# Kernel tuning notes

Measured on AMD Instinct MI355X. Metric: run time of the kernel, lower is better.

## Reference

```python
import jax, jax.numpy as jnp
import numpy as np
from jax import lax

FEAT_STRIDE = 16
RATIOS = np.array([0.5, 1.0, 2.0], np.float32)
SCALES = np.array([8.0, 16.0, 32.0], np.float32)
PRE_NMS, POST_NMS = 6000, 300
NMS_THRESH, MIN_SIZE, SCALE = 0.7, 16.0, 1.0


def anchor_base():
    py = px = FEAT_STRIDE / 2.0
    base = np.zeros((9, 4), np.float32)
    for i, r in enumerate(RATIOS):
        for j, s in enumerate(SCALES):
            h = FEAT_STRIDE * s * np.sqrt(r)
            w = FEAT_STRIDE * s * np.sqrt(1.0 / r)
            base[i * 3 + j] = [px - w / 2.0, py - h / 2.0, px + w / 2.0, py + h / 2.0]
    return jnp.asarray(base)


def all_anchors(h, w):
    base = anchor_base()  # (9,4)
    sy = jnp.arange(h, dtype=jnp.float32) * FEAT_STRIDE
    sx = jnp.arange(w, dtype=jnp.float32) * FEAT_STRIDE
    yy, xx = jnp.meshgrid(sy, sx, indexing='ij')
    shift = jnp.stack([xx.ravel(), yy.ravel(), xx.ravel(), yy.ravel()], axis=1)  # (hw,4)
    return (shift[:, None, :] + base[None, :, :]).reshape(-1, 4)  # (hw*9,4)


def conv2d(x, w, b):
    y = lax.conv_general_dilated(x, w, (1, 1), 'SAME',
                                 dimension_numbers=('NCHW', 'OIHW', 'NCHW'))
    return y + b[None, :, None, None]


def loc2bbox(anchor, loc):
    aw = anchor[:, 2] - anchor[:, 0]
    ah = anchor[:, 3] - anchor[:, 1]
    ax = anchor[:, 0] + 0.5 * aw
    ay = anchor[:, 1] + 0.5 * ah
    cx = loc[:, 0] * aw + ax
    cy = loc[:, 1] * ah + ay
    w = jnp.exp(loc[:, 2]) * aw
    h = jnp.exp(loc[:, 3]) * ah
    return jnp.stack([cx - 0.5 * w, cy - 0.5 * h, cx + 0.5 * w, cy + 0.5 * h], axis=1)


def nms_fixed(boxes, scores):
    # top pre_nms by score, then greedy sequential NMS with fixed shapes
    s, order = lax.top_k(scores, PRE_NMS)
    b = boxes[order]
    areas = (b[:, 2] - b[:, 0]) * (b[:, 3] - b[:, 1])
    idx = jnp.arange(PRE_NMS)

    def body(i, keep):
        xx1 = jnp.maximum(b[i, 0], b[:, 0])
        yy1 = jnp.maximum(b[i, 1], b[:, 1])
        xx2 = jnp.minimum(b[i, 2], b[:, 2])
        yy2 = jnp.minimum(b[i, 3], b[:, 3])
        inter = jnp.clip(xx2 - xx1, 0.0) * jnp.clip(yy2 - yy1, 0.0)
        iou = inter / (areas[i] + areas - inter + 1e-9)
        suppress = (iou > NMS_THRESH) & (idx > i) & keep[i]
        return keep & ~suppress

    keep = lax.fori_loop(0, PRE_NMS, body, jnp.isfinite(s))
    vals, sel = lax.top_k(jnp.where(keep, s, -jnp.inf), POST_NMS)
    roi = b[sel]
    return jnp.where(jnp.isfinite(vals)[:, None], roi, 0.0)  # (POST_NMS,4)


def proposal(loc, fg, anchor, img_h, img_w):
    roi = loc2bbox(anchor, loc)
    roi = jnp.stack([jnp.clip(roi[:, 0], 0.0, img_w), jnp.clip(roi[:, 1], 0.0, img_h),
                     jnp.clip(roi[:, 2], 0.0, img_w), jnp.clip(roi[:, 3], 0.0, img_h)], axis=1)
    ms = MIN_SIZE * SCALE
    valid = ((roi[:, 2] - roi[:, 0]) >= ms) & ((roi[:, 3] - roi[:, 1]) >= ms)
    return nms_fixed(roi, jnp.where(valid, fg, -jnp.inf))


def setup_inputs() -> dict:
    key = jax.random.key(0)
    ks = jax.random.split(key, 4)
    return {
        'x': jax.random.normal(ks[0], (8, 512, 50, 76), jnp.float32),
        'conv1_w': jax.random.normal(ks[1], (512, 512, 3, 3), jnp.float32) * 0.01,
        'conv1_b': jnp.zeros((512,), jnp.float32),
        'score_w': jax.random.normal(ks[2], (18, 512, 1, 1), jnp.float32) * 0.01,
        'score_b': jnp.zeros((18,), jnp.float32),
        'loc_w': jax.random.normal(ks[3], (36, 512, 1, 1), jnp.float32) * 0.01,
        'loc_b': jnp.zeros((36,), jnp.float32),
        'img_h': 800,
        'img_w': 1216,
    }


def reference(x, conv1_w, conv1_b, score_w, score_b, loc_w, loc_b, img_h, img_w):
    b, c, h, w = x.shape
    anchor = all_anchors(h, w)  # (h*w*9,4)
    feat = jax.nn.relu(conv2d(x, conv1_w, conv1_b))
    rpn_locs = conv2d(feat, loc_w, loc_b).transpose(0, 2, 3, 1).reshape(b, -1, 4)
    rpn_scores = conv2d(feat, score_w, score_b).transpose(0, 2, 3, 1)
    sm = jax.nn.softmax(rpn_scores.reshape(b, h, w, 9, 2), axis=4)
    fg = sm[..., 1].reshape(b, -1)
    rpn_scores = rpn_scores.reshape(b, -1, 2)
    rois = jax.vmap(lambda l, f: proposal(l, f, anchor, float(img_h), float(img_w)))(rpn_locs, fg)
    rois = rois.reshape(-1, 4)  # (b*POST_NMS,4)
    return rpn_locs, rpn_scores, rois, anchor
```

## Files before the change

kernel.cpp:

```cpp
#include <hip/hip_runtime.h>
#include <stdint.h>
#include <math.h>

typedef unsigned long long u64;
typedef unsigned int u32;
typedef _Float16 half8 __attribute__((ext_vector_type(8)));
typedef float f32x4 __attribute__((ext_vector_type(4)));

#define CC   512
#define HH   50
#define WW2  76
#define PP   3800
#define NB   8
#define NA   34200
#define PRE  6000
#define POST 300
#define MWORDS 96
#define NPAD 8192
#define SHALF 4096
#define SCHUNK 1069


__device__ __forceinline__ u32 skey(float f) {
    u32 u = __float_as_uint(f);
    return (u & 0x80000000u) ? ~u : (u | 0x80000000u);
}

__device__ __forceinline__ float4 anchor_at(int p, int a) {
    const float rv[3] = {0.5f, 1.0f, 2.0f};
    const float sv[3] = {8.0f, 16.0f, 32.0f};
    int ri = a / 3, si = a % 3;
    float s16 = 16.0f * sv[si];
    float hh = s16 * sqrtf(rv[ri]);
    float ww = s16 * sqrtf(1.0f / rv[ri]);
    float bx1 = 8.0f - 0.5f * ww, by1 = 8.0f - 0.5f * hh;
    float bx2 = 8.0f + 0.5f * ww, by2 = 8.0f + 0.5f * hh;
    float sx = (float)((p % WW2) * 16);
    float sy = (float)((p / WW2) * 16);
    return make_float4(sx + bx1, sy + by1, sx + bx2, sy + by2);
}

__device__ __forceinline__ int lds_slot(int m, int j) {
    return (((m >> 4) * 64) + ((m & 15) ^ ((4 * (j & 1)) | (8 * (j >> 1)))) + (j << 4)) << 3;
}

__global__ void k_split_x(const float* __restrict__ x, _Float16* __restrict__ xh,
                          _Float16* __restrict__ xl) {
    __shared__ float S[32][33];
    int zim = blockIdx.z;
    int p0 = blockIdx.x * 32, c0 = blockIdx.y * 32;
    int tx = threadIdx.x, ty0 = threadIdx.y;
    const float* xi = x + (size_t)zim * CC * PP;
#pragma unroll
    for (int yy = 0; yy < 32; yy += 8) {
        int cty = c0 + ty0 + yy, ptx = p0 + tx;
        S[ty0 + yy][tx] = (ptx < PP) ? xi[(size_t)cty * PP + ptx] : 0.f;
    }
    __syncthreads();
#pragma unroll
    for (int yy = 0; yy < 32; yy += 8) {
        int p = p0 + ty0 + yy;
        if (p < PP) {
            float v = S[tx][ty0 + yy];
            _Float16 h = (_Float16)v;
            float r = v - (float)h;
            size_t o = (size_t)(zim * PP + p) * 512 + c0 + tx;
            xh[o] = h;
            xl[o] = (_Float16)(r * 2048.0f);
        }
    }
}

__global__ void k_split_w(const float* __restrict__ w, _Float16* __restrict__ wh,
                          _Float16* __restrict__ wl) {
    __shared__ float S[4608];
    int co = blockIdx.x;
    for (int t = threadIdx.x; t < 4608; t += 256) S[t] = w[(size_t)co * 4608 + t];
    __syncthreads();
    int g = co >> 4, nlo = co & 15;
    for (int e = threadIdx.x; e < 4608; e += 256) {
        int cc = e / 9, idx = e - cc * 9;
        float v = S[cc * 9 + idx];
        _Float16 h = (_Float16)v;
        float r = v - (float)h;
        int kk = (cc >> 5) * 9 + idx;
        int lane = ((cc >> 3) & 3) * 16 + nlo;
        int j = cc & 7;
        size_t d = (((size_t)g * 144 + kk) * 64 + lane) * 8 + j;
        wh[d] = h;
        wl[d] = (_Float16)(r * 2048.0f);
    }
}

__global__ void k_split_w2(const float* __restrict__ lw, const float* __restrict__ sw,
                           _Float16* __restrict__ wh2, _Float16* __restrict__ wl2) {
    int row = blockIdx.x, k = threadIdx.x;
    float v = (row < 36) ? lw[row * 512 + k] : (row < 54 ? sw[(row - 36) * 512 + k] : 0.f);
    _Float16 h = (_Float16)v;
    float r = v - (float)h;
    wh2[row * 512 + k] = h;
    wl2[row * 512 + k] = (_Float16)(r * 2048.0f);
}

__global__ __launch_bounds__(256, 2) void k_conv(
    const _Float16* __restrict__ xh, const _Float16* __restrict__ xl,
    const _Float16* __restrict__ whF, const _Float16* __restrict__ wlF,
    const float* __restrict__ bias, _Float16* __restrict__ fh,
    _Float16* __restrict__ fl, int imgbase)
{
    __shared__ _Float16 lds[2 * 8192];
    const int tid = threadIdx.x;
    const int L = blockIdx.x;
    const int X = L & 7, q = L >> 3;
    const int nt = X & 3;
    const int zim = (X >> 2) * 2 + (q >= 30 ? 1 : 0);
    const int mt = q - (q >= 30 ? 30 : 0);
    const int m0 = mt * 128, n0 = nt * 128;
    const _Float16* xhi = xh + (size_t)zim * CC * PP;
    const _Float16* xlo = xl + (size_t)zim * CC * PP;

    const int mA0 = tid >> 2, jA0 = tid & 3;
    const int mA1 = 64 + (tid >> 2);

    f32x4 acc[4][4], acc2[4][4];
#pragma unroll
    for (int i = 0; i < 4; ++i)
#pragma unroll
        for (int j = 0; j < 4; ++j) {
            acc[i][j] = f32x4{0.f, 0.f, 0.f, 0.f};
            acc2[i][j] = f32x4{0.f, 0.f, 0.f, 0.f};
        }

    uint4 pa0h, pa0l, pa1h, pa1l;

    auto ld_a = [&](int m, int idx, int c0, uint4& vh, uint4& vl) {
        int dy = idx / 3 - 1, dx = idx % 3 - 1;
        int p = m0 + m;
        int px = p % 76, py = p / 76;
        bool av = (p < PP) && ((unsigned)(py + dy) < 50u) && ((unsigned)(px + dx) < 76u);
        if (av) {
            size_t off = (size_t)(p + dy * 76 + dx) * 512 + c0 + jA0 * 8;
            vh = *(const uint4*)(xhi + off);
            vl = *(const uint4*)(xlo + off);
        } else {
            vh = make_uint4(0, 0, 0, 0);
            vl = make_uint4(0, 0, 0, 0);
        }
    };
    auto stage_load = [&](int kk) {
        int c9 = kk / 9;
        int idx = kk - c9 * 9;
        int c0 = c9 << 5;
        ld_a(mA0, idx, c0, pa0h, pa0l);
        ld_a(mA1, idx, c0, pa1h, pa1l);
    };
    const int sl0 = lds_slot(mA0, jA0);
    const int sl1 = lds_slot(mA1, jA0);
    auto stage_write = [&](int buf) {
        _Float16* Lp = lds + buf * 8192;
        *(uint4*)(Lp + sl0)        = pa0h;
        *(uint4*)(Lp + 4096 + sl0) = pa0l;
        *(uint4*)(Lp + sl1)        = pa1h;
        *(uint4*)(Lp + 4096 + sl1) = pa1l;
    };

    const int lane = tid & 63, wave = tid >> 6;
    const int wm = wave & 1, wn = wave >> 1;
    const int jr = lane >> 4;
    const int rd_off = (((lane & 15) ^ ((4 * (jr & 1)) | (8 * (jr >> 1)))) + (jr << 4)) << 3;
    const int g0 = nt * 8 + wn * 4;
    const size_t lane8 = (size_t)lane * 8;

    half8 b0h[4], b0l[4], b1h[4], b1l[4];
    auto load_b = [&](int kk, half8* bh_, half8* bl_) {
#pragma unroll
        for (int ni = 0; ni < 4; ++ni) {
            size_t off = (((size_t)(g0 + ni) * 144 + kk) * 64) * 8 + lane8;
            bh_[ni] = *(const half8*)(whF + off);
            bl_[ni] = *(const half8*)(wlF + off);
        }
    };

    auto compute = [&](int buf, const half8* bh, const half8* bl) {
        const _Float16* Lp = lds + buf * 8192;
        half8 ah[4], al[4];
#pragma unroll
        for (int mi = 0; mi < 4; ++mi) {
            int slot = (((wm * 4 + mi) * 64) << 3) + rd_off;
            ah[mi] = *(const half8*)(Lp + slot);
            al[mi] = *(const half8*)(Lp + 4096 + slot);
        }
#pragma unroll
        for (int ni = 0; ni < 4; ++ni) {
#pragma unroll
            for (int mi = 0; mi < 4; ++mi) {
                acc[mi][ni]  = __builtin_amdgcn_mfma_f32_16x16x32_f16(ah[mi], bh[ni], acc[mi][ni], 0, 0, 0);
                acc2[mi][ni] = __builtin_amdgcn_mfma_f32_16x16x32_f16(ah[mi], bl[ni], acc2[mi][ni], 0, 0, 0);
                acc2[mi][ni] = __builtin_amdgcn_mfma_f32_16x16x32_f16(al[mi], bh[ni], acc2[mi][ni], 0, 0, 0);
            }
        }
    };

    stage_load(0);
    stage_write(0);
    load_b(0, b0h, b0l);
    __syncthreads();
    for (int kk = 0; kk < 144; kk += 2) {
        stage_load(kk + 1);
        load_b(kk + 1, b1h, b1l);
        compute(0, b0h, b0l);
        stage_write(1);
        __syncthreads();
        if (kk + 2 < 144) {
            stage_load(kk + 2);
            load_b(kk + 2, b0h, b0l);
        }
        compute(1, b1h, b1l);
        if (kk + 2 < 144) stage_write(0);
        __syncthreads();
    }

    const int qq = lane >> 4, cl = lane & 15;
    const size_t rowbase = (size_t)(imgbase + zim) * PP;
#pragma unroll
    for (int ni = 0; ni < 4; ++ni) {
        int n = n0 + (wn * 4 + ni) * 16 + cl;
        float bs = bias[n];
#pragma unroll
        for (int mi = 0; mi < 4; ++mi) {
            int mb = m0 + (wm * 4 + mi) * 16 + qq * 4;
            if (mb < PP) {
#pragma unroll
                for (int r = 0; r < 4; ++r) {
                    float v = fmaxf(acc[mi][ni][r] + acc2[mi][ni][r] * (1.f / 2048.f) + bs, 0.f);
                    _Float16 h = (_Float16)v;
                    float rr = v - (float)h;
                    size_t o = (rowbase + mb + r) * 512 + n;
                    fh[o] = h;
                    fl[o] = (_Float16)(rr * 2048.0f);
                }
            }
        }
    }
}

__global__ __launch_bounds__(256) void k_hgemm_post(
    const _Float16* __restrict__ fh, const _Float16* __restrict__ fl,
    const _Float16* __restrict__ wh2, const _Float16* __restrict__ wl2,
    const float* __restrict__ lb, const float* __restrict__ sbias,
    const int* __restrict__ imh_p, const int* __restrict__ imw_p,
    float* __restrict__ out0, float* __restrict__ out1,
    float* __restrict__ boxes, float* __restrict__ scores,
    float* __restrict__ out3)
{
    const int img = blockIdx.y;
    const int p0 = blockIdx.x * 64;
    const int wave = threadIdx.x >> 6, lane = threadIdx.x & 63;
    const int q8 = (lane >> 4) * 8;
    int arow = img * PP + p0 + wave * 16 + (lane & 15);
    if (arow >= NB * PP) arow = NB * PP - 1;
    const _Float16* fhp = fh + (size_t)arow * 512 + q8;
    const _Float16* flp = fl + (size_t)arow * 512 + q8;
    const _Float16* bhp = wh2 + (size_t)(lane & 15) * 512 + q8;
    const _Float16* blp = wl2 + (size_t)(lane & 15) * 512 + q8;

    f32x4 acc[4], acc2[4];
#pragma unroll
    for (int j = 0; j < 4; ++j) {
        acc[j] = f32x4{0.f, 0.f, 0.f, 0.f};
        acc2[j] = f32x4{0.f, 0.f, 0.f, 0.f};
    }

#pragma unroll 4
    for (int k0 = 0; k0 < 512; k0 += 32) {
        half8 ah = *(const half8*)(fhp + k0);
        half8 al = *(const half8*)(flp + k0);
#pragma unroll
        for (int nf = 0; nf < 4; ++nf) {
            half8 bh = *(const half8*)(bhp + (size_t)nf * 16 * 512 + k0);
            half8 bl = *(const half8*)(blp + (size_t)nf * 16 * 512 + k0);
            acc[nf]  = __builtin_amdgcn_mfma_f32_16x16x32_f16(ah, bh, acc[nf], 0, 0, 0);
            acc2[nf] = __builtin_amdgcn_mfma_f32_16x16x32_f16(ah, bl, acc2[nf], 0, 0, 0);
            acc2[nf] = __builtin_amdgcn_mfma_f32_16x16x32_f16(al, bh, acc2[nf], 0, 0, 0);
        }
    }

    __shared__ float Ls[64][68];
    const int q = lane >> 4, cl = lane & 15;
#pragma unroll
    for (int nf = 0; nf < 4; ++nf) {
        int n = nf * 16 + cl;
        float bs = (n < 36) ? lb[n] : (n < 54 ? sbias[n - 36] : 0.f);
#pragma unroll
        for (int r = 0; r < 4; ++r) {
            int ml = wave * 16 + q * 4 + r;
            Ls[ml][n] = acc[nf][r] + acc2[nf][r] * (1.f / 2048.f) + bs;
        }
    }
    __syncthreads();

    const float fimh = (float)(*imh_p), fimw = (float)(*imw_p);
    for (int task = threadIdx.x; task < 576; task += 256) {
        int pl = task / 9, a = task - pl * 9;
        int p = p0 + pl;
        if (p >= PP) continue;
        float4 loc = *(const float4*)&Ls[pl][a * 4];
        float2 sc = make_float2(Ls[pl][36 + a * 2], Ls[pl][36 + a * 2 + 1]);
        size_t ai = (size_t)img * NA + (size_t)p * 9 + a;
        *(float4*)&out0[ai * 4] = loc;
        *(float2*)&out1[ai * 2] = sc;
        float mx = fmaxf(sc.x, sc.y);
        float e0 = expf(sc.x - mx), e1 = expf(sc.y - mx);
        float fg = e1 / (e0 + e1);
        float4 an = anchor_at(p, a);
        if (img == 0) ((float4*)out3)[p * 9 + a] = an;
        float aw = an.z - an.x, ah = an.w - an.y;
        float ax = an.x + 0.5f * aw, ay = an.y + 0.5f * ah;
        float cx = loc.x * aw + ax;
        float cy = loc.y * ah + ay;
        float wb = expf(loc.z) * aw, hb = expf(loc.w) * ah;
        float x1 = cx - 0.5f * wb, y1 = cy - 0.5f * hb;
        float x2 = cx + 0.5f * wb, y2 = cy + 0.5f * hb;
        x1 = fminf(fmaxf(x1, 0.f), fimw);
        x2 = fminf(fmaxf(x2, 0.f), fimw);
        y1 = fminf(fmaxf(y1, 0.f), fimh);
        y2 = fminf(fmaxf(y2, 0.f), fimh);
        bool valid = ((x2 - x1) >= 16.0f) && ((y2 - y1) >= 16.0f);
        ((float4*)boxes)[ai] = make_float4(x1, y1, x2, y2);
        scores[ai] = valid ? fg : -INFINITY;
    }
}


__global__ __launch_bounds__(256) void k_sel_hist(
    const float* __restrict__ scores, u32* __restrict__ ghist,
    const u32* __restrict__ gpref, int sh, int pass)
{
    __shared__ u32 wh[4][256];
    const int img = blockIdx.y, blk = blockIdx.x;
    const int tid = threadIdx.x, wv = tid >> 6;
#pragma unroll
    for (int w = 0; w < 4; ++w) wh[w][tid] = 0;
    __syncthreads();
    const u32 pmask = (pass == 0) ? 0u : (0xFFFFFFFFu << (sh + 8));
    const u32 pref = (pass == 0) ? 0u : gpref[img];
    const float4* sc4 = (const float4*)(scores + (size_t)img * NA);
    const int e40 = blk * SCHUNK;
    const int e41 = min(e40 + SCHUNK, NA / 4);
    for (int e4 = e40 + tid; e4 < e41; e4 += 256) {
        float4 s4 = sc4[e4];
        u32 kv[4] = {skey(s4.x), skey(s4.y), skey(s4.z), skey(s4.w)};
#pragma unroll
        for (int v = 0; v < 4; ++v)
            if ((kv[v] & pmask) == pref) atomicAdd(&wh[wv][(kv[v] >> sh) & 255u], 1u);
    }
    __syncthreads();
    u32 s = wh[0][tid] + wh[1][tid] + wh[2][tid] + wh[3][tid];
    if (s) atomicAdd(&ghist[img * 256 + tid], s);
}

__global__ __launch_bounds__(256) void k_sel_scan(
    u32* __restrict__ ghist, u32* __restrict__ gpref, u32* __restrict__ grem,
    int sh, int pass)
{
    __shared__ u32 A[256];
    __shared__ int s_d;
    const int img = blockIdx.x, t = threadIdx.x;
    u32 h = ghist[img * 256 + t];
    A[t] = h;
    if (t == 0) s_d = 0;
    __syncthreads();
    for (int off = 1; off < 256; off <<= 1) {
        u32 v = A[t] + ((t + off < 256) ? A[t + off] : 0u);
        __syncthreads();
        A[t] = v;
        __syncthreads();
    }
    const u32 rem = (pass == 0) ? (u32)PRE : grem[img];
    if (A[t] >= rem) atomicMax(&s_d, t);
    __syncthreads();
    if (t == 0) {
        int d = s_d;
        u32 snext = (d < 255) ? A[d + 1] : 0u;
        u32 pv = (pass == 0) ? 0u : gpref[img];
        gpref[img] = pv | ((u32)d << sh);
        grem[img] = rem - snext;
    }
    ghist[img * 256 + t] = 0;
}

__global__ __launch_bounds__(256) void k_sel_collect(
    const float* __restrict__ scores, const u32* __restrict__ gpref,
    u32* __restrict__ gccnt, u64* __restrict__ arr)
{
    __shared__ u64 lst[4288];
    __shared__ u32 s_c, s_base;
    const int img = blockIdx.y, blk = blockIdx.x;
    const int tid = threadIdx.x, lane = tid & 63;
    if (tid == 0) s_c = 0;
    __syncthreads();
    const u32 T = gpref[img];
    const float4* sc4 = (const float4*)(scores + (size_t)img * NA);
    const int e40 = blk * SCHUNK;
    const int e41 = min(e40 + SCHUNK, NA / 4);
    for (int e4 = e40 + tid; e4 < e41; e4 += 256) {
        float4 s4 = sc4[e4];
        u32 ks[4] = {skey(s4.x), skey(s4.y), skey(s4.z), skey(s4.w)};
#pragma unroll
        for (int v = 0; v < 4; ++v) {
            bool take = ks[v] >= T;
            u64 bal = __ballot(take);
            if (bal) {
                int leader = __builtin_ctzll(bal);
                u32 base = 0;
                if (lane == leader) base = atomicAdd(&s_c, (u32)__popcll(bal));
                base = (u32)__shfl((int)base, leader);
                if (take)
                    lst[base + (u32)__popcll(bal & ((1ull << lane) - 1ull))] =
                        ((u64)ks[v] << 32) | (u64)(~(u32)(e4 * 4 + v));
            }
        }
    }
    __syncthreads();
    if (tid == 0) s_base = atomicAdd(&gccnt[img], s_c);
    __syncthreads();
    const u32 base = s_base, c = s_c;
    u64* ar = arr + (size_t)img * NPAD;
    for (u32 t = tid; t < c; t += 256) {
        u32 pos = base + t;
        if (pos < NPAD) ar[pos] = lst[t];
    }
}

__global__ __launch_bounds__(1024) void k_sel_sort2(
    u64* __restrict__ arr, const u32* __restrict__ gccnt)
{
    __shared__ u64 a[SHALF];
    const int img = blockIdx.y, half = blockIdx.x;
    const int tid = threadIdx.x;
    u32 n = gccnt[img]; if (n > NPAD) n = NPAD;
    u64* ar = arr + (size_t)img * NPAD + (size_t)half * SHALF;
    const int base = half * SHALF;
    for (int t = tid; t < SHALF; t += 1024)
        a[t] = ((u32)(base + t) < n) ? ar[t] : 0ull;
    for (u32 size = 2; size <= SHALF; size <<= 1) {
        for (u32 stride = size >> 1; stride > 0; stride >>= 1) {
            __syncthreads();
            for (u32 t2 = tid; t2 < SHALF / 2; t2 += 1024) {
                u32 i = 2 * t2 - (t2 & (stride - 1));
                u32 j = i + stride;
                u64 x = a[i], y = a[j];
                bool desc = ((i & size) == 0);
                if (desc ? (x < y) : (x > y)) { a[i] = y; a[j] = x; }
            }
        }
    }
    __syncthreads();
    for (int t = tid; t < SHALF; t += 1024) ar[t] = a[t];
}

__global__ __launch_bounds__(1024) void k_sel_merge(
    const float* __restrict__ scores, const float4* __restrict__ boxes,
    const u64* __restrict__ arr,
    float* __restrict__ sb, float4* __restrict__ bbs, float* __restrict__ areas)
{
    const int img = blockIdx.y;
    const int t = blockIdx.x * 1024 + threadIdx.x;
    if (t >= PRE) return;
    const u64* A = arr + (size_t)img * NPAD;
    const u64* B = A + SHALF;
    int lo = (t > SHALF) ? (t - SHALF) : 0;
    int hi = (t < SHALF) ? t : SHALF;
    while (lo < hi) {
        int mid = (lo + hi) >> 1;
        if (A[mid] > B[t - 1 - mid]) lo = mid + 1; else hi = mid;
    }
    const int i = lo, j = t - lo;
    u64 va = (i < SHALF) ? A[i] : 0ull;
    u64 vb = (j < SHALF) ? B[j] : 0ull;
    u64 v = (va > vb) ? va : vb;
    u32 e = ~(u32)v;
    const float* sc = scores + (size_t)img * NA;
    float s = sc[e];
    float4 bx = boxes[(size_t)img * NA + e];
    sb[img * PRE + t] = s;
    bbs[img * PRE + t] = bx;
    areas[img * PRE + t] = (bx.z - bx.x) * (bx.w - bx.y);
}

__global__ __launch_bounds__(256) void k_mask(
    const float4* __restrict__ bbs, const float* __restrict__ areas,
    u64* __restrict__ mask)
{
    int img = blockIdx.z, iT = blockIdx.x, jT = blockIdx.y;
    if (jT * 256 + 255 <= iT * 64) return;
    int tid = threadIdx.x;
    __shared__ float4 jb[256];
    __shared__ float ja[256];
    int jj = jT * 256 + tid;
    jb[tid] = (jj < PRE) ? bbs[(size_t)img * PRE + jj] : make_float4(0, 0, 0, 0);
    ja[tid] = (jj < PRE) ? areas[img * PRE + jj] : 0.f;
    __syncthreads();
    int i = iT * 64 + (tid & 63);
    int jw = jT * 4 + (tid >> 6);
    if (i >= PRE) return;
    float4 bi = bbs[(size_t)img * PRE + i];
    float ai = areas[img * PRE + i];
    int j0 = (tid >> 6) * 64;
    u64 m = 0;
#pragma unroll 4
    for (int b = 0; b < 64; ++b) {
        int j = jw * 64 + b;
        if (j >= PRE) break;
        if (j > i) {
            float4 bj = jb[j0 + b];
            float xx1 = fmaxf(bi.x, bj.x), yy1 = fmaxf(bi.y, bj.y);
            float xx2 = fminf(bi.z, bj.z), yy2 = fminf(bi.w, bj.w);
            float iw = fmaxf(xx2 - xx1, 0.f), ih2 = fmaxf(yy2 - yy1, 0.f);
            float inter = iw * ih2;
            float iou = inter / (ai + ja[j0 + b] - inter + 1e-9f);
            if (iou > 0.7f) m |= (1ull << b);
        }
    }
    mask[((size_t)img * PRE + i) * MWORDS + jw] = m;
}

__global__ __launch_bounds__(256) void k_scan(
    const float* __restrict__ sb, const float4* __restrict__ bbs,
    const u64* __restrict__ mask, float* __restrict__ out2)
{
    const int img = blockIdx.x;
    const int tid = threadIdx.x;
    const int lane = tid & 63, wv = tid >> 6;
    __shared__ u64 alive[94];
    __shared__ int list[POST];
    __shared__ int s_n;
    __shared__ u64 wred[4];

    for (int j0 = 0; j0 < 94 * 64; j0 += 256) {
        int j = j0 + tid;
        bool al = (j < PRE) && isfinite(sb[(size_t)img * PRE + j]);
        u64 bal = __ballot(al);
        if (lane == 0) alive[(j0 >> 6) + wv] = bal;
    }
    if (tid == 0) s_n = 0;
    __syncthreads();

    const u64* mimg = mask + (size_t)img * PRE * MWORDS;
    for (int w = 0; w < 94; ++w) {
        int n = s_n;
        if (n >= POST) break;
        u64 myrow = 0;
        if (wv == 0) myrow = mimg[(size_t)(w * 64 + lane) * MWORDS + w];
        u64 loc = 0;
        for (int t = tid; t < n; t += 256)
            loc |= mimg[(size_t)list[t] * MWORDS + w];
#pragma unroll
        for (int off = 32; off > 0; off >>= 1)
            loc |= __shfl_down(loc, off);
        if (lane == 0) wred[wv] = loc;
        __syncthreads();
        if (wv == 0) {
            u64 supp = wred[0] | wred[1] | wred[2] | wred[3];
            u64 cur = alive[w] & ~supp;
            u64 keptw = 0;
            while (cur) {
                int b = __builtin_ctzll(cur);
                keptw |= 1ull << b;
                u64 row = __shfl(myrow, b);
                u64 hi = (b >= 63) ? 0ull : (~0ull << (b + 1));
                cur &= ~row & hi;
            }
            if (lane == 0) {
                int nn = n;
                u64 bits = keptw;
                while (bits && nn < POST) {
                    int bb = __builtin_ctzll(bits);
                    bits &= bits - 1;
                    list[nn++] = w * 64 + bb;
                }
                s_n = nn;
            }
        }
        __syncthreads();
    }
    __syncthreads();
    int n = s_n;
    for (int e = tid; e < POST; e += 256) {
        float4 bx = (e < n) ? bbs[(size_t)img * PRE + list[e]] : make_float4(0, 0, 0, 0);
        *(float4*)&out2[((size_t)img * POST + e) * 4] = bx;
    }
}

extern "C" void kernel_launch(void* const* d_in, const int* in_sizes, int n_in,
                              void* d_out, int out_size, void* d_ws, size_t ws_size,
                              hipStream_t stream)
{
    const float* x     = (const float*)d_in[0];
    const float* w1    = (const float*)d_in[1];
    const float* b1    = (const float*)d_in[2];
    const float* sw    = (const float*)d_in[3];
    const float* sbias = (const float*)d_in[4];
    const float* lw    = (const float*)d_in[5];
    const float* lb    = (const float*)d_in[6];
    const int*   imh   = (const int*)d_in[7];
    const int*   imw   = (const int*)d_in[8];
    float* out = (float*)d_out;
    char* ws = (char*)d_ws;

    _Float16* wh2W = (_Float16*)(ws + 0);
    _Float16* wl2W = (_Float16*)(ws + 65536);
    _Float16* whW  = (_Float16*)(ws + 131072);
    _Float16* wlW  = (_Float16*)(ws + 4849664);
    _Float16* xhW  = (_Float16*)(ws + 9568256);
    _Float16* xlW  = (_Float16*)(ws + 25133056);
    float*    boxesW  = (float*)(ws + 17350656);
    float*    scoresW = (float*)(ws + 21728256);
    float*    sbW     = (float*)(ws + 22822656);
    float*    bbsW    = (float*)(ws + 23014656);
    float*    areasW  = (float*)(ws + 23782656);
    _Float16* fhW  = (_Float16*)(ws + 40697856);
    _Float16* flW  = (_Float16*)(ws + 71827456);
    u64*      maskW   = (u64*)(ws + 40697856);
    u32*      ghistW  = (u32*)(ws + 109581056);
    u32*      gccntW  = (u32*)(ws + 109589248);
    u32*      gprefW  = (u32*)(ws + 109589280);
    u32*      gremW   = (u32*)(ws + 109589312);
    u64*      arrW    = (u64*)(ws + 109597440);

    float* out0 = out;
    float* out1 = out + 1094400;
    float* out2 = out + 1641600;
    float* out3 = out + 1651200;

    hipMemsetAsync(ws + 109581056, 0, 8224, stream);

    hipLaunchKernelGGL(k_split_w, dim3(512), dim3(256), 0, stream, w1, whW, wlW);
    hipLaunchKernelGGL(k_split_w2, dim3(64), dim3(512), 0, stream, lw, sw, wh2W, wl2W);
    for (int b = 0; b < 2; ++b) {
        hipLaunchKernelGGL(k_split_x, dim3(119, 16, 4), dim3(32, 8), 0, stream,
                           x + (size_t)b * 4 * CC * PP, xhW, xlW);
        hipLaunchKernelGGL(k_conv, dim3(480), dim3(256), 0, stream,
                           xhW, xlW, whW, wlW, b1, fhW, flW, b * 4);
    }
    hipLaunchKernelGGL(k_hgemm_post, dim3(60, NB), dim3(256), 0, stream,
                       fhW, flW, wh2W, wl2W, lb, sbias, imh, imw,
                       out0, out1, boxesW, scoresW, out3);
    for (int pass = 0; pass < 4; ++pass) {
        int sh = 24 - 8 * pass;
        hipLaunchKernelGGL(k_sel_hist, dim3(8, NB), dim3(256), 0, stream,
                           scoresW, ghistW, gprefW, sh, pass);
        hipLaunchKernelGGL(k_sel_scan, dim3(NB), dim3(256), 0, stream,
                           ghistW, gprefW, gremW, sh, pass);
    }
    hipLaunchKernelGGL(k_sel_collect, dim3(8, NB), dim3(256), 0, stream,
                       scoresW, gprefW, gccntW, arrW);
    hipLaunchKernelGGL(k_sel_sort2, dim3(2, NB), dim3(1024), 0, stream,
                       arrW, gccntW);
    hipLaunchKernelGGL(k_sel_merge, dim3((PRE + 1023) / 1024, NB), dim3(1024), 0, stream,
                       scoresW, (const float4*)boxesW, arrW,
                       sbW, (float4*)bbsW, areasW);
    hipLaunchKernelGGL(k_mask, dim3(94, 24, NB), dim3(256), 0, stream,
                       (const float4*)bbsW, areasW, maskW);
    hipLaunchKernelGGL(k_scan, dim3(NB), dim3(256), 0, stream,
                       sbW, (const float4*)bbsW, maskW, out2);
}
```

Measured before the change: 863.8 us.

## Compute NMS IoU lazily in scan, fuse selection hist/scan and weight splits

```diff
diff --git a/kernel.cpp b/kernel.cpp
--- a/kernel.cpp
+++ b/kernel.cpp
@@ -15,7 +15,6 @@
 #define NA   34200
 #define PRE  6000
 #define POST 300
-#define MWORDS 96
 #define NPAD 8192
 #define SHALF 4096
 #define SCHUNK 1069
@@ -71,8 +70,22 @@
     }
 }
 
-__global__ void k_split_w(const float* __restrict__ w, _Float16* __restrict__ wh,
-                          _Float16* __restrict__ wl) {
+__global__ void k_split_wall(const float* __restrict__ w, _Float16* __restrict__ wh,
+                             _Float16* __restrict__ wl,
+                             const float* __restrict__ lw, const float* __restrict__ sw,
+                             _Float16* __restrict__ wh2, _Float16* __restrict__ wl2) {
+    if (blockIdx.x >= 512) {
+        int row = blockIdx.x - 512;
+        for (int k = threadIdx.x; k < 512; k += 256) {
+            float v = (row < 36) ? lw[row * 512 + k]
+                                 : (row < 54 ? sw[(row - 36) * 512 + k] : 0.f);
+            _Float16 h = (_Float16)v;
+            float r = v - (float)h;
+            wh2[row * 512 + k] = h;
+            wl2[row * 512 + k] = (_Float16)(r * 2048.0f);
+        }
+        return;
+    }
     __shared__ float S[4608];
     int co = blockIdx.x;
     for (int t = threadIdx.x; t < 4608; t += 256) S[t] = w[(size_t)co * 4608 + t];
@@ -90,16 +103,6 @@
         wh[d] = h;
         wl[d] = (_Float16)(r * 2048.0f);
     }
-}
-
-__global__ void k_split_w2(const float* __restrict__ lw, const float* __restrict__ sw,
-                           _Float16* __restrict__ wh2, _Float16* __restrict__ wl2) {
-    int row = blockIdx.x, k = threadIdx.x;
-    float v = (row < 36) ? lw[row * 512 + k] : (row < 54 ? sw[(row - 36) * 512 + k] : 0.f);
-    _Float16 h = (_Float16)v;
-    float r = v - (float)h;
-    wh2[row * 512 + k] = h;
-    wl2[row * 512 + k] = (_Float16)(r * 2048.0f);
 }
 
 __global__ __launch_bounds__(256, 2) void k_conv(
@@ -332,11 +335,14 @@
 }
 
 
-__global__ __launch_bounds__(256) void k_sel_hist(
+__global__ __launch_bounds__(256) void k_sel_histscan(
     const float* __restrict__ scores, u32* __restrict__ ghist,
-    const u32* __restrict__ gpref, int sh, int pass)
+    u32* __restrict__ gpref, u32* __restrict__ grem, u32* __restrict__ gdone,
+    int sh, int pass)
 {
     __shared__ u32 wh[4][256];
+    __shared__ u32 A[256];
+    __shared__ int s_last, s_d;
     const int img = blockIdx.y, blk = blockIdx.x;
     const int tid = threadIdx.x, wv = tid >> 6;
 #pragma unroll
@@ -357,36 +363,32 @@
     __syncthreads();
     u32 s = wh[0][tid] + wh[1][tid] + wh[2][tid] + wh[3][tid];
     if (s) atomicAdd(&ghist[img * 256 + tid], s);
-}
-
-__global__ __launch_bounds__(256) void k_sel_scan(
-    u32* __restrict__ ghist, u32* __restrict__ gpref, u32* __restrict__ grem,
-    int sh, int pass)
-{
-    __shared__ u32 A[256];
-    __shared__ int s_d;
-    const int img = blockIdx.x, t = threadIdx.x;
-    u32 h = ghist[img * 256 + t];
-    A[t] = h;
-    if (t == 0) s_d = 0;
+    __threadfence();
+    __syncthreads();
+    if (tid == 0) s_last = (atomicAdd(&gdone[pass * 8 + img], 1u) == 7u) ? 1 : 0;
+    __syncthreads();
+    if (!s_last) return;
+    u32 h = atomicAdd(&ghist[img * 256 + tid], 0u);
+    A[tid] = h;
+    if (tid == 0) s_d = 0;
     __syncthreads();
     for (int off = 1; off < 256; off <<= 1) {
-        u32 v = A[t] + ((t + off < 256) ? A[t + off] : 0u);
+        u32 v = A[tid] + ((tid + off < 256) ? A[tid + off] : 0u);
         __syncthreads();
-        A[t] = v;
+        A[tid] = v;
         __syncthreads();
     }
     const u32 rem = (pass == 0) ? (u32)PRE : grem[img];
-    if (A[t] >= rem) atomicMax(&s_d, t);
-    __syncthreads();
-    if (t == 0) {
+    if (A[tid] >= rem) atomicMax(&s_d, tid);
+    __syncthreads();
+    if (tid == 0) {
         int d = s_d;
         u32 snext = (d < 255) ? A[d + 1] : 0u;
         u32 pv = (pass == 0) ? 0u : gpref[img];
         gpref[img] = pv | ((u32)d << sh);
         grem[img] = rem - snext;
     }
-    ghist[img * 256 + t] = 0;
+    ghist[img * 256 + tid] = 0;
 }
 
 __global__ __launch_bounds__(256) void k_sel_collect(
@@ -488,54 +490,22 @@
     areas[img * PRE + t] = (bx.z - bx.x) * (bx.w - bx.y);
 }
 
-__global__ __launch_bounds__(256) void k_mask(
-    const float4* __restrict__ bbs, const float* __restrict__ areas,
-    u64* __restrict__ mask)
-{
-    int img = blockIdx.z, iT = blockIdx.x, jT = blockIdx.y;
-    if (jT * 256 + 255 <= iT * 64) return;
-    int tid = threadIdx.x;
-    __shared__ float4 jb[256];
-    __shared__ float ja[256];
-    int jj = jT * 256 + tid;
-    jb[tid] = (jj < PRE) ? bbs[(size_t)img * PRE + jj] : make_float4(0, 0, 0, 0);
-    ja[tid] = (jj < PRE) ? areas[img * PRE + jj] : 0.f;
-    __syncthreads();
-    int i = iT * 64 + (tid & 63);
-    int jw = jT * 4 + (tid >> 6);
-    if (i >= PRE) return;
-    float4 bi = bbs[(size_t)img * PRE + i];
-    float ai = areas[img * PRE + i];
-    int j0 = (tid >> 6) * 64;
-    u64 m = 0;
-#pragma unroll 4
-    for (int b = 0; b < 64; ++b) {
-        int j = jw * 64 + b;
-        if (j >= PRE) break;
-        if (j > i) {
-            float4 bj = jb[j0 + b];
-            float xx1 = fmaxf(bi.x, bj.x), yy1 = fmaxf(bi.y, bj.y);
-            float xx2 = fminf(bi.z, bj.z), yy2 = fminf(bi.w, bj.w);
-            float iw = fmaxf(xx2 - xx1, 0.f), ih2 = fmaxf(yy2 - yy1, 0.f);
-            float inter = iw * ih2;
-            float iou = inter / (ai + ja[j0 + b] - inter + 1e-9f);
-            if (iou > 0.7f) m |= (1ull << b);
-        }
-    }
-    mask[((size_t)img * PRE + i) * MWORDS + jw] = m;
-}
-
 __global__ __launch_bounds__(256) void k_scan(
     const float* __restrict__ sb, const float4* __restrict__ bbs,
-    const u64* __restrict__ mask, float* __restrict__ out2)
+    float* __restrict__ out2)
 {
     const int img = blockIdx.x;
     const int tid = threadIdx.x;
     const int lane = tid & 63, wv = tid >> 6;
     __shared__ u64 alive[94];
     __shared__ int list[POST];
+    __shared__ float4 kb[POST];
+    __shared__ float ka[POST];
+    __shared__ float4 wb4[64];
+    __shared__ float wa[64];
+    __shared__ u64 rowp[4][64];
+    __shared__ u64 wred[4];
     __shared__ int s_n;
-    __shared__ u64 wred[4];
 
     for (int j0 = 0; j0 < 94 * 64; j0 += 256) {
         int j = j0 + tid;
@@ -546,15 +516,51 @@
     if (tid == 0) s_n = 0;
     __syncthreads();
 
-    const u64* mimg = mask + (size_t)img * PRE * MWORDS;
     for (int w = 0; w < 94; ++w) {
         int n = s_n;
         if (n >= POST) break;
-        u64 myrow = 0;
-        if (wv == 0) myrow = mimg[(size_t)(w * 64 + lane) * MWORDS + w];
+        if (tid < 64) {
+            int j = w * 64 + tid;
+            float4 b = (j < PRE) ? bbs[(size_t)img * PRE + j] : make_float4(0, 0, 0, 0);
+            wb4[tid] = b;
+            wa[tid] = (b.z - b.x) * (b.w - b.y);
+        }
+        __syncthreads();
+        {
+            int l = tid & 63, part = tid >> 6;
+            float4 bl = wb4[l];
+            float al_ = wa[l];
+            u64 m = 0;
+            int b0 = part * 16;
+#pragma unroll 4
+            for (int b = b0; b < b0 + 16; ++b) {
+                float4 bj = wb4[b];
+                float xx1 = fmaxf(bl.x, bj.x), yy1 = fmaxf(bl.y, bj.y);
+                float xx2 = fminf(bl.z, bj.z), yy2 = fminf(bl.w, bj.w);
+                float iw = fmaxf(xx2 - xx1, 0.f), ih2 = fmaxf(yy2 - yy1, 0.f);
+                float inter = iw * ih2;
+                float iou = inter / (al_ + wa[b] - inter + 1e-9f);
+                if (iou > 0.7f) m |= (1ull << b);
+            }
+            rowp[part][l] = m;
+        }
         u64 loc = 0;
-        for (int t = tid; t < n; t += 256)
-            loc |= mimg[(size_t)list[t] * MWORDS + w];
+        for (int t = tid; t < n; t += 256) {
+            float4 kbx = kb[t];
+            float kar = ka[t];
+            u64 m = 0;
+#pragma unroll 4
+            for (int b = 0; b < 64; ++b) {
+                float4 bj = wb4[b];
+                float xx1 = fmaxf(kbx.x, bj.x), yy1 = fmaxf(kbx.y, bj.y);
+                float xx2 = fminf(kbx.z, bj.z), yy2 = fminf(kbx.w, bj.w);
+                float iw = fmaxf(xx2 - xx1, 0.f), ih2 = fmaxf(yy2 - yy1, 0.f);
+                float inter = iw * ih2;
+                float iou = inter / (kar + wa[b] - inter + 1e-9f);
+                if (iou > 0.7f) m |= (1ull << b);
+            }
+            loc |= m;
+        }
 #pragma unroll
         for (int off = 32; off > 0; off >>= 1)
             loc |= __shfl_down(loc, off);
@@ -562,6 +568,7 @@
         __syncthreads();
         if (wv == 0) {
             u64 supp = wred[0] | wred[1] | wred[2] | wred[3];
+            u64 myrow = rowp[0][lane] | rowp[1][lane] | rowp[2][lane] | rowp[3][lane];
             u64 cur = alive[w] & ~supp;
             u64 keptw = 0;
             while (cur) {
@@ -577,7 +584,10 @@
                 while (bits && nn < POST) {
                     int bb = __builtin_ctzll(bits);
                     bits &= bits - 1;
-                    list[nn++] = w * 64 + bb;
+                    list[nn] = w * 64 + bb;
+                    kb[nn] = wb4[bb];
+                    ka[nn] = wa[bb];
+                    ++nn;
                 }
                 s_n = nn;
             }
@@ -621,11 +631,11 @@
     float*    areasW  = (float*)(ws + 23782656);
     _Float16* fhW  = (_Float16*)(ws + 40697856);
     _Float16* flW  = (_Float16*)(ws + 71827456);
-    u64*      maskW   = (u64*)(ws + 40697856);
     u32*      ghistW  = (u32*)(ws + 109581056);
     u32*      gccntW  = (u32*)(ws + 109589248);
     u32*      gprefW  = (u32*)(ws + 109589280);
     u32*      gremW   = (u32*)(ws + 109589312);
+    u32*      gdoneW  = (u32*)(ws + 109589344);
     u64*      arrW    = (u64*)(ws + 109597440);
 
     float* out0 = out;
@@ -633,10 +643,10 @@
     float* out2 = out + 1641600;
     float* out3 = out + 1651200;
 
-    hipMemsetAsync(ws + 109581056, 0, 8224, stream);
-
-    hipLaunchKernelGGL(k_split_w, dim3(512), dim3(256), 0, stream, w1, whW, wlW);
-    hipLaunchKernelGGL(k_split_w2, dim3(64), dim3(512), 0, stream, lw, sw, wh2W, wl2W);
+    hipMemsetAsync(ws + 109581056, 0, 8416, stream);
+
+    hipLaunchKernelGGL(k_split_wall, dim3(576), dim3(256), 0, stream,
+                       w1, whW, wlW, lw, sw, wh2W, wl2W);
     for (int b = 0; b < 2; ++b) {
         hipLaunchKernelGGL(k_split_x, dim3(119, 16, 4), dim3(32, 8), 0, stream,
                            x + (size_t)b * 4 * CC * PP, xhW, xlW);
@@ -648,10 +658,8 @@
                        out0, out1, boxesW, scoresW, out3);
     for (int pass = 0; pass < 4; ++pass) {
         int sh = 24 - 8 * pass;
-        hipLaunchKernelGGL(k_sel_hist, dim3(8, NB), dim3(256), 0, stream,
-                           scoresW, ghistW, gprefW, sh, pass);
-        hipLaunchKernelGGL(k_sel_scan, dim3(NB), dim3(256), 0, stream,
-                           ghistW, gprefW, gremW, sh, pass);
+        hipLaunchKernelGGL(k_sel_histscan, dim3(8, NB), dim3(256), 0, stream,
+                           scoresW, ghistW, gprefW, gremW, gdoneW, sh, pass);
     }
     hipLaunchKernelGGL(k_sel_collect, dim3(8, NB), dim3(256), 0, stream,
                        scoresW, gprefW, gccntW, arrW);
@@ -660,8 +668,6 @@
     hipLaunchKernelGGL(k_sel_merge, dim3((PRE + 1023) / 1024, NB), dim3(1024), 0, stream,
                        scoresW, (const float4*)boxesW, arrW,
                        sbW, (float4*)bbsW, areasW);
-    hipLaunchKernelGGL(k_mask, dim3(94, 24, NB), dim3(256), 0, stream,
-                       (const float4*)bbsW, areasW, maskW);
     hipLaunchKernelGGL(k_scan, dim3(NB), dim3(256), 0, stream,
-                       sbW, (const float4*)bbsW, maskW, out2);
-}
+                       sbW, (const float4*)bbsW, out2);
+}
```

Result: faster. 821.9 us, median of 2 (-4.8%).
